# Optimization experiments

Hardware: AMD Instinct MI355X
Metric: run time of the kernel (lower is better)

The kernel has to match this reference:

```python
import jax, jax.numpy as jnp
import numpy as np

N = 50000          # nodes
E = 1600000        # edges
H = 8              # heads
F = 16             # out feats per head (np1class)
IN = 256           # in feats
NEG_SLOPE = 0.2    # DGL GATConv default leaky_relu slope


def setup_inputs() -> dict:
    key = jax.random.key(0)
    ks = jax.random.split(key, 7)
    x = jax.random.normal(ks[0], (N, IN), dtype=jnp.float32)
    W = jax.random.normal(ks[1], (IN, H * F), dtype=jnp.float32) * 0.05
    attn_l = jax.random.normal(ks[2], (H, F), dtype=jnp.float32) * 0.05
    attn_r = jax.random.normal(ks[3], (H, F), dtype=jnp.float32) * 0.05
    bias = jax.random.normal(ks[4], (H * F,), dtype=jnp.float32) * 0.05
    src = jax.random.randint(ks[5], (E,), 0, N, dtype=jnp.int64)
    dst = jax.random.randint(ks[6], (E,), 0, N, dtype=jnp.int64)
    return {"x": x, "W": W, "attn_l": attn_l, "attn_r": attn_r,
            "bias": bias, "src": src, "dst": dst}


def reference(x, W, attn_l, attn_r, bias, src, dst):
    # Linear projection to heads: [N, H, F]
    feat = (x @ W).reshape(N, H, F)
    # Per-node attention halves: [N, H]
    el = jnp.einsum('nhf,hf->nh', feat, attn_l)
    er = jnp.einsum('nhf,hf->nh', feat, attn_r)
    # Edge scores: e = leaky_relu(el[src] + er[dst])  -> [E, H]
    e = jax.nn.leaky_relu(el[src] + er[dst], negative_slope=NEG_SLOPE)
    # Segment softmax over incoming edges of each destination node
    m = jax.ops.segment_max(e, dst, num_segments=N)           # [N, H]
    m = jnp.where(jnp.isfinite(m), m, 0.0)                    # empty segments
    m = jax.lax.stop_gradient(m)
    ex = jnp.exp(e - m[dst])                                  # [E, H]
    s = jax.ops.segment_sum(ex, dst, num_segments=N)          # [N, H]
    a = ex / jnp.maximum(s[dst], 1e-9)                        # [E, H]
    # Weighted aggregation of source features: [N, H, F]
    msg = a[:, :, None] * feat[src]
    rst = jax.ops.segment_sum(msg, dst, num_segments=N)
    rst = rst + bias.reshape(H, F)
    # Classifier: mean over heads -> [N, F]
    return rst.mean(axis=1)
```

## Files before the change

kernel.cpp:

```cpp
#include <hip/hip_runtime.h>
#include <hip/hip_bf16.h>

#define NH 8
#define NF 16
#define NIN 256
#define HF 128
#define CAP 3072

typedef __attribute__((ext_vector_type(8))) short bf16x8;
typedef __attribute__((ext_vector_type(4))) float f32x4;

__device__ __forceinline__ unsigned short f2bf(float f) {
    union { float f; unsigned int u; } v; v.f = f;
    unsigned int r = v.u + 0x7FFFu + ((v.u >> 16) & 1u);
    return (unsigned short)(r >> 16);
}
__device__ __forceinline__ float bf2f(unsigned short b) {
    union { unsigned int u; float f; } v; v.u = ((unsigned int)b) << 16;
    return v.f;
}

#define GROWS 128
__global__ __launch_bounds__(256) void gemm_mfma(const float* __restrict__ A,
                                                 const float* __restrict__ W,
                                                 const float* __restrict__ attn_l,
                                                 const float* __restrict__ attn_r,
                                                 unsigned short* __restrict__ featb,
                                                 float* __restrict__ el,
                                                 float* __restrict__ er, int M) {
    __shared__ unsigned short AsH[32][264];
    __shared__ unsigned short AsL[32][264];
    const int tid = threadIdx.x;
    const int wave = tid >> 6, lane = tid & 63;
    const int quad = lane >> 4, lq = lane & 15;
    const int row0 = blockIdx.x * GROWS;

    bf16x8 bfrag[8][2];
#pragma unroll
    for (int h2 = 0; h2 < 2; h2++) {
        const int col = (wave * 2 + h2) * 16 + lq;
#pragma unroll
        for (int kk = 0; kk < 8; kk++) {
            const int kb = kk * 32 + quad * 8;
            bf16x8 f;
#pragma unroll
            for (int j = 0; j < 8; j++)
                f[j] = (short)f2bf(W[(size_t)(kb + j) * HF + col]);
            bfrag[kk][h2] = f;
        }
    }
    const float al0 = attn_l[(wave * 2 + 0) * 16 + lq];
    const float al1 = attn_l[(wave * 2 + 1) * 16 + lq];
    const float ar0 = attn_r[(wave * 2 + 0) * 16 + lq];
    const float ar1 = attn_r[(wave * 2 + 1) * 16 + lq];

    const int srow = tid >> 3;

    for (int c = 0; c < 4; c++) {
        const int crow0 = row0 + c * 32;
        __syncthreads();
#pragma unroll
        for (int i = 0; i < 8; i++) {
            const int col = ((tid & 7) + i * 8) * 4;
            const int gr = crow0 + srow;
            float4 v = make_float4(0.f, 0.f, 0.f, 0.f);
            if (gr < M) v = *(const float4*)&A[(size_t)gr * NIN + col];
            const unsigned short h0 = f2bf(v.x), h1 = f2bf(v.y),
                                 h2b = f2bf(v.z), h3 = f2bf(v.w);
            *(ushort4*)&AsH[srow][col] = make_ushort4(h0, h1, h2b, h3);
            *(ushort4*)&AsL[srow][col] =
                make_ushort4(f2bf(v.x - bf2f(h0)), f2bf(v.y - bf2f(h1)),
                             f2bf(v.z - bf2f(h2b)), f2bf(v.w - bf2f(h3)));
        }
        __syncthreads();
#pragma unroll
        for (int s = 0; s < 2; s++) {
            f32x4 acc0 = {0.f, 0.f, 0.f, 0.f};
            f32x4 acc1 = {0.f, 0.f, 0.f, 0.f};
            const int ar = s * 16 + lq;
#pragma unroll
            for (int kk = 0; kk < 8; kk++) {
                const bf16x8 ah = *(const bf16x8*)&AsH[ar][kk * 32 + quad * 8];
                const bf16x8 al = *(const bf16x8*)&AsL[ar][kk * 32 + quad * 8];
                acc0 = __builtin_amdgcn_mfma_f32_16x16x32_bf16(ah, bfrag[kk][0], acc0, 0, 0, 0);
                acc1 = __builtin_amdgcn_mfma_f32_16x16x32_bf16(ah, bfrag[kk][1], acc1, 0, 0, 0);
                acc0 = __builtin_amdgcn_mfma_f32_16x16x32_bf16(al, bfrag[kk][0], acc0, 0, 0, 0);
                acc1 = __builtin_amdgcn_mfma_f32_16x16x32_bf16(al, bfrag[kk][1], acc1, 0, 0, 0);
            }
#pragma unroll
            for (int r = 0; r < 4; r++) {
                const int gr = crow0 + s * 16 + quad * 4 + r;
                float pl0 = acc0[r] * al0, pr0 = acc0[r] * ar0;
                float pl1 = acc1[r] * al1, pr1 = acc1[r] * ar1;
#pragma unroll
                for (int m = 1; m < 16; m <<= 1) {
                    pl0 += __shfl_xor(pl0, m, 64);
                    pr0 += __shfl_xor(pr0, m, 64);
                    pl1 += __shfl_xor(pl1, m, 64);
                    pr1 += __shfl_xor(pr1, m, 64);
                }
                if (gr < M) {
                    featb[(size_t)gr * HF + (wave * 2 + 0) * 16 + lq] = f2bf(acc0[r]);
                    featb[(size_t)gr * HF + (wave * 2 + 1) * 16 + lq] = f2bf(acc1[r]);
                    if (lq == 0) {
                        el[(size_t)gr * NH + wave * 2 + 0] = pl0;
                        el[(size_t)gr * NH + wave * 2 + 1] = pl1;
                        er[(size_t)gr * NH + wave * 2 + 0] = pr0;
                        er[(size_t)gr * NH + wave * 2 + 1] = pr1;
                    }
                }
            }
        }
    }
}

#define BCH 16384
__global__ __launch_bounds__(256) void bin_kernel(const int* __restrict__ src,
                                                  const int* __restrict__ dst,
                                                  int* __restrict__ bcnt,
                                                  unsigned int* __restrict__ binned,
                                                  int E, int NB) {
    __shared__ unsigned int hist[800];
    __shared__ unsigned short lpos[BCH];
    const int tid = threadIdx.x;
    const int base = blockIdx.x * BCH;
    for (int b = tid; b < NB; b += 256) hist[b] = 0;
    __syncthreads();
    const int cnt = min(BCH, E - base);
    for (int i = tid; i < cnt; i += 256) {
        const int b = dst[base + i] >> 6;
        lpos[i] = (unsigned short)atomicAdd(&hist[b], 1u);
    }
    __syncthreads();
    for (int b = tid; b < NB; b += 256) {
        const unsigned int c = hist[b];
        if (c) hist[b] = (unsigned int)(b * CAP + atomicAdd(&bcnt[b], (int)c));
    }
    __syncthreads();
    for (int i = tid; i < cnt; i += 256) {
        const int d = dst[base + i];
        const int b = d >> 6;
        const unsigned int pos = hist[b] + (unsigned int)lpos[i];
        binned[pos] = (unsigned int)src[base + i] | ((unsigned int)(d & 63) << 16);
    }
}

__global__ __launch_bounds__(1024) void bscan_kernel(const int* __restrict__ bcnt,
                                                     int* __restrict__ bbase,
                                                     int* __restrict__ rowptr,
                                                     int NB, int N, int E) {
    __shared__ int wsum[16];
    const int t = threadIdx.x, lane = t & 63, w = t >> 6;
    const int v = (t < NB) ? bcnt[t] : 0;
    int incl = v;
#pragma unroll
    for (int off = 1; off < 64; off <<= 1) {
        const int x = __shfl_up(incl, off, 64);
        if (lane >= off) incl += x;
    }
    if (lane == 63) wsum[w] = incl;
    __syncthreads();
    int wbase = 0;
    for (int k = 0; k < w; k++) wbase += wsum[k];
    if (t < NB) bbase[t] = wbase + incl - v;
    if (t == 0) rowptr[N] = E;
}

__global__ __launch_bounds__(256) void csr_kernel(const int* __restrict__ bcnt,
                                                  const int* __restrict__ bbase,
                                                  const unsigned int* __restrict__ binned,
                                                  int* __restrict__ rowptr,
                                                  int* __restrict__ srcs, int N) {
    __shared__ int cnt64[64];
    __shared__ int cur[64];
    const int b = blockIdx.x, t = threadIdx.x;
    const int node0 = b << 6;
    const int cntb = bcnt[b];
    const unsigned int* bb = &binned[(size_t)b * CAP];
    if (t < 64) cnt64[t] = 0;
    __syncthreads();
    for (int i = t; i < cntb; i += 256) atomicAdd(&cnt64[bb[i] >> 16], 1);
    __syncthreads();
    if (t < 64) {
        const int v = cnt64[t];
        int incl = v;
#pragma unroll
        for (int off = 1; off < 64; off <<= 1) {
            const int x = __shfl_up(incl, off, 64);
            if (t >= off) incl += x;
        }
        const int excl = bbase[b] + incl - v;
        if (node0 + t < N) rowptr[node0 + t] = excl;
        cur[t] = excl;
    }
    __syncthreads();
    for (int i = t; i < cntb; i += 256) {
        const unsigned int p = bb[i];
        const int pos = atomicAdd(&cur[p >> 16], 1);
        srcs[pos] = (int)(p & 0xFFFFu);
    }
}

__global__ __launch_bounds__(128) void agg_kernel(const int* __restrict__ rowptr,
                                                  const int* __restrict__ srcs,
                                                  const float* __restrict__ el,
                                                  const float* __restrict__ er,
                                                  const unsigned short* __restrict__ featb,
                                                  const float* __restrict__ bias,
                                                  float* __restrict__ out) {
    const int n = blockIdx.x;
    const int tid = threadIdx.x;
    __shared__ float lds_sc[32][8];
    __shared__ int lds_src[32];
    __shared__ float lds_ps[128];
    __shared__ float lds_s[8];
    __shared__ float2 lds_acc[2][64];
    __shared__ float2 lds_v[8][8];

    const int begin = rowptr[n], end = rowptr[n + 1];
    const int hA = tid & 7, eA = tid >> 3;
    const float er_h = er[(size_t)n * NH + hA];
    const int w = tid >> 6, lane = tid & 63;
    const int hB = lane >> 3, fB2 = lane & 7;

    float2 acc = make_float2(0.f, 0.f);
    float psum = 0.f;
    for (int base = begin; base < end; base += 32) {
        const int cn = min(32, end - base);
#pragma unroll
        for (int rep = 0; rep < 2; rep++) {
            const int ei = eA + rep * 16;
            if (ei < cn) {
                const int si = srcs[base + ei];
                if (hA == 0) lds_src[ei] = si;
                float v = el[(size_t)si * NH + hA] + er_h;
                v = v > 0.f ? v : 0.2f * v;
                const float sc = __expf(v);
                lds_sc[ei][hA] = sc;
                psum += sc;
            }
        }
        __syncthreads();
        unsigned int fv[16];
#pragma unroll
        for (int j = 0; j < 16; j++) {
            const int ej = w * 16 + j;
            const int sj = lds_src[ej];
            fv[j] = (ej < cn)
                        ? *(const unsigned int*)&featb[(size_t)sj * HF + hB * 16 + fB2 * 2]
                        : 0u;
        }
#pragma unroll
        for (int j = 0; j < 16; j++) {
            const int ej = w * 16 + j;
            const float sc = (ej < cn) ? lds_sc[ej][hB] : 0.f;
            acc.x = fmaf(sc, bf2f((unsigned short)(fv[j] & 0xFFFFu)), acc.x);
            acc.y = fmaf(sc, bf2f((unsigned short)(fv[j] >> 16)), acc.y);
        }
        __syncthreads();
    }

    lds_ps[tid] = psum;
    lds_acc[w][lane] = acc;
    __syncthreads();
    if (tid < 8) {
        float s = 0.f;
#pragma unroll
        for (int k = 0; k < 16; k++) s += lds_ps[k * 8 + tid];
        lds_s[tid] = fmaxf(s, 1e-9f);
    }
    __syncthreads();
    if (tid < 64) {
        const float2 t0 = lds_acc[0][tid], t1 = lds_acc[1][tid];
        const float inv = 1.f / lds_s[hB];
        float2 val;
        val.x = (t0.x + t1.x) * inv + bias[hB * 16 + fB2 * 2];
        val.y = (t0.y + t1.y) * inv + bias[hB * 16 + fB2 * 2 + 1];
        lds_v[hB][fB2] = val;
    }
    __syncthreads();
    if (tid < 8) {
        float2 o = make_float2(0.f, 0.f);
#pragma unroll
        for (int h = 0; h < 8; h++) {
            const float2 v = lds_v[h][tid];
            o.x += v.x; o.y += v.y;
        }
        o.x *= 0.125f; o.y *= 0.125f;
        *(float2*)&out[(size_t)n * 16 + tid * 2] = o;
    }
}

extern "C" void kernel_launch(void* const* d_in, const int* in_sizes, int n_in,
                              void* d_out, int out_size, void* d_ws, size_t ws_size,
                              hipStream_t stream) {
    const float* x      = (const float*)d_in[0];
    const float* W      = (const float*)d_in[1];
    const float* attn_l = (const float*)d_in[2];
    const float* attn_r = (const float*)d_in[3];
    const float* bias   = (const float*)d_in[4];
    const int*   src    = (const int*)d_in[5];
    const int*   dst    = (const int*)d_in[6];
    float* out = (float*)d_out;

    const int N = in_sizes[0] / NIN;
    const int E = in_sizes[5];
    const int NB = (N + 63) >> 6;

    char* w = (char*)d_ws;
    unsigned short* featb = (unsigned short*)w; w += (size_t)N * HF * 2;
    float* el     = (float*)w; w += (size_t)N * NH * 4;
    float* er     = (float*)w; w += (size_t)N * NH * 4;
    int* rowptr   = (int*)w;   w += (size_t)(N + 16) * 4;
    int* bcnt     = (int*)w;   w += (size_t)((NB + 15) & ~15) * 4;
    int* bbase    = (int*)w;   w += (size_t)((NB + 15) & ~15) * 4;
    unsigned int* binned = (unsigned int*)w; w += (size_t)NB * CAP * 4;
    int* srcs     = (int*)w;

    hipMemsetAsync(bcnt, 0, (size_t)NB * sizeof(int), stream);

    gemm_mfma<<<(N + GROWS - 1) / GROWS, 256, 0, stream>>>(x, W, attn_l, attn_r,
                                                           featb, el, er, N);
    bin_kernel<<<(E + BCH - 1) / BCH, 256, 0, stream>>>(src, dst, bcnt, binned, E, NB);
    bscan_kernel<<<1, 1024, 0, stream>>>(bcnt, bbase, rowptr, NB, N, E);
    csr_kernel<<<NB, 256, 0, stream>>>(bcnt, bbase, binned, rowptr, srcs, N);
    agg_kernel<<<N, 128, 0, stream>>>(rowptr, srcs, el, er, featb, bias, out);
}
```

Measured before the change: 260.3 us.

## Fuse CSR construction into aggregation; one block per 64-node bin

Removes the global scan and CSR kernels. Each aggregation block now takes one 64-node bin, builds a local per-node sort of source indices in shared memory, and loops over its 64 nodes serially with 256 threads. The bin chunk size also shrinks, which gives more binning blocks. This saves two launches and the global srcs/rowptr round trip, but the grid drops from 50000 blocks to about 782. Each block processes its nodes one after another with many barriers, so latency hiding for the featb gathers may suffer.

Result: slower. 344.1 us (+32.2%).

```diff
diff --git a/kernel.cpp b/kernel.cpp
--- a/kernel.cpp
+++ b/kernel.cpp
@@ -6,6 +6,7 @@
 #define NIN 256
 #define HF 128
 #define CAP 3072
+#define BCH 4096
 
 typedef __attribute__((ext_vector_type(8))) short bf16x8;
 typedef __attribute__((ext_vector_type(4))) float f32x4;
@@ -114,7 +115,6 @@
     }
 }
 
-#define BCH 16384
 __global__ __launch_bounds__(256) void bin_kernel(const int* __restrict__ src,
                                                   const int* __restrict__ dst,
                                                   int* __restrict__ bcnt,
@@ -145,149 +145,136 @@
     }
 }
 
-__global__ __launch_bounds__(1024) void bscan_kernel(const int* __restrict__ bcnt,
-                                                     int* __restrict__ bbase,
-                                                     int* __restrict__ rowptr,
-                                                     int NB, int N, int E) {
-    __shared__ int wsum[16];
-    const int t = threadIdx.x, lane = t & 63, w = t >> 6;
-    const int v = (t < NB) ? bcnt[t] : 0;
-    int incl = v;
-#pragma unroll
-    for (int off = 1; off < 64; off <<= 1) {
-        const int x = __shfl_up(incl, off, 64);
-        if (lane >= off) incl += x;
-    }
-    if (lane == 63) wsum[w] = incl;
-    __syncthreads();
-    int wbase = 0;
-    for (int k = 0; k < w; k++) wbase += wsum[k];
-    if (t < NB) bbase[t] = wbase + incl - v;
-    if (t == 0) rowptr[N] = E;
-}
-
-__global__ __launch_bounds__(256) void csr_kernel(const int* __restrict__ bcnt,
-                                                  const int* __restrict__ bbase,
+__global__ __launch_bounds__(256) void agg_kernel(const int* __restrict__ bcnt,
                                                   const unsigned int* __restrict__ binned,
-                                                  int* __restrict__ rowptr,
-                                                  int* __restrict__ srcs, int N) {
-    __shared__ int cnt64[64];
-    __shared__ int cur[64];
-    const int b = blockIdx.x, t = threadIdx.x;
-    const int node0 = b << 6;
-    const int cntb = bcnt[b];
-    const unsigned int* bb = &binned[(size_t)b * CAP];
-    if (t < 64) cnt64[t] = 0;
-    __syncthreads();
-    for (int i = t; i < cntb; i += 256) atomicAdd(&cnt64[bb[i] >> 16], 1);
-    __syncthreads();
-    if (t < 64) {
-        const int v = cnt64[t];
-        int incl = v;
-#pragma unroll
-        for (int off = 1; off < 64; off <<= 1) {
-            const int x = __shfl_up(incl, off, 64);
-            if (t >= off) incl += x;
-        }
-        const int excl = bbase[b] + incl - v;
-        if (node0 + t < N) rowptr[node0 + t] = excl;
-        cur[t] = excl;
-    }
-    __syncthreads();
-    for (int i = t; i < cntb; i += 256) {
-        const unsigned int p = bb[i];
-        const int pos = atomicAdd(&cur[p >> 16], 1);
-        srcs[pos] = (int)(p & 0xFFFFu);
-    }
-}
-
-__global__ __launch_bounds__(128) void agg_kernel(const int* __restrict__ rowptr,
-                                                  const int* __restrict__ srcs,
                                                   const float* __restrict__ el,
                                                   const float* __restrict__ er,
                                                   const unsigned short* __restrict__ featb,
                                                   const float* __restrict__ bias,
-                                                  float* __restrict__ out) {
-    const int n = blockIdx.x;
-    const int tid = threadIdx.x;
-    __shared__ float lds_sc[32][8];
-    __shared__ int lds_src[32];
-    __shared__ float lds_ps[128];
-    __shared__ float lds_s[8];
-    __shared__ float2 lds_acc[2][64];
-    __shared__ float2 lds_v[8][8];
-
-    const int begin = rowptr[n], end = rowptr[n + 1];
-    const int hA = tid & 7, eA = tid >> 3;
-    const float er_h = er[(size_t)n * NH + hA];
-    const int w = tid >> 6, lane = tid & 63;
+                                                  float* __restrict__ out, int N) {
+    const int b = blockIdx.x, t = threadIdx.x;
+    const int node0 = b << 6;
+    __shared__ unsigned short sSrc[CAP];
+    __shared__ int len64[64], base64[64], cur64[64];
+    __shared__ float er_lds[64][NH];
+    __shared__ float lds_sc[32][NH];
+    __shared__ float lds_ps[256];
+    __shared__ float lds_s[NH];
+    __shared__ float2 lds_acc[4][64];
+    __shared__ float2 lds_v[NH][8];
+
+    const int cntb = bcnt[b];
+    const unsigned int* bb = &binned[(size_t)b * CAP];
+
+    if (t < 64) len64[t] = 0;
+    __syncthreads();
+    for (int i = t; i < cntb; i += 256) atomicAdd(&len64[bb[i] >> 16], 1);
+    __syncthreads();
+    if (t < 64) {
+        const int v = len64[t];
+        int incl = v;
+#pragma unroll
+        for (int off = 1; off < 64; off <<= 1) {
+            const int x = __shfl_up(incl, off, 64);
+            if (t >= off) incl += x;
+        }
+        base64[t] = incl - v;
+        cur64[t] = incl - v;
+    }
+    {
+        const int lim = min(64 * NH, (N - node0) * NH);
+        __syncthreads();
+        for (int i = t; i < lim; i += 256)
+            ((float*)er_lds)[i] = er[(size_t)node0 * NH + i];
+    }
+    __syncthreads();
+    for (int i = t; i < cntb; i += 256) {
+        const unsigned int p = bb[i];
+        const int pos = atomicAdd(&cur64[p >> 16], 1);
+        sSrc[pos] = (unsigned short)(p & 0xFFFFu);
+    }
+    __syncthreads();
+
+    const int hA = t & 7, eA = t >> 3;
+    const int w = t >> 6, lane = t & 63;
     const int hB = lane >> 3, fB2 = lane & 7;
 
-    float2 acc = make_float2(0.f, 0.f);
-    float psum = 0.f;
-    for (int base = begin; base < end; base += 32) {
-        const int cn = min(32, end - base);
-#pragma unroll
-        for (int rep = 0; rep < 2; rep++) {
-            const int ei = eA + rep * 16;
-            if (ei < cn) {
-                const int si = srcs[base + ei];
-                if (hA == 0) lds_src[ei] = si;
+    const int nmax = min(64, N - node0);
+    for (int nl = 0; nl < nmax; nl++) {
+        const int begin = base64[nl];
+        const int lenn = len64[nl];
+        const float er_h = er_lds[nl][hA];
+        float2 acc = make_float2(0.f, 0.f);
+        float psum = 0.f;
+        for (int base = begin; base < begin + lenn; base += 32) {
+            const int cn = min(32, begin + lenn - base);
+            if (eA < cn) {
+                const int si = sSrc[base + eA];
                 float v = el[(size_t)si * NH + hA] + er_h;
                 v = v > 0.f ? v : 0.2f * v;
                 const float sc = __expf(v);
-                lds_sc[ei][hA] = sc;
+                lds_sc[eA][hA] = sc;
                 psum += sc;
             }
-        }
-        __syncthreads();
-        unsigned int fv[16];
-#pragma unroll
-        for (int j = 0; j < 16; j++) {
-            const int ej = w * 16 + j;
-            const int sj = lds_src[ej];
-            fv[j] = (ej < cn)
-                        ? *(const unsigned int*)&featb[(size_t)sj * HF + hB * 16 + fB2 * 2]
-                        : 0u;
-        }
-#pragma unroll
-        for (int j = 0; j < 16; j++) {
-            const int ej = w * 16 + j;
-            const float sc = (ej < cn) ? lds_sc[ej][hB] : 0.f;
-            acc.x = fmaf(sc, bf2f((unsigned short)(fv[j] & 0xFFFFu)), acc.x);
-            acc.y = fmaf(sc, bf2f((unsigned short)(fv[j] >> 16)), acc.y);
-        }
-        __syncthreads();
-    }
-
-    lds_ps[tid] = psum;
-    lds_acc[w][lane] = acc;
-    __syncthreads();
-    if (tid < 8) {
-        float s = 0.f;
-#pragma unroll
-        for (int k = 0; k < 16; k++) s += lds_ps[k * 8 + tid];
-        lds_s[tid] = fmaxf(s, 1e-9f);
-    }
-    __syncthreads();
-    if (tid < 64) {
-        const float2 t0 = lds_acc[0][tid], t1 = lds_acc[1][tid];
-        const float inv = 1.f / lds_s[hB];
-        float2 val;
-        val.x = (t0.x + t1.x) * inv + bias[hB * 16 + fB2 * 2];
-        val.y = (t0.y + t1.y) * inv + bias[hB * 16 + fB2 * 2 + 1];
-        lds_v[hB][fB2] = val;
-    }
-    __syncthreads();
-    if (tid < 8) {
-        float2 o = make_float2(0.f, 0.f);
-#pragma unroll
-        for (int h = 0; h < 8; h++) {
-            const float2 v = lds_v[h][tid];
-            o.x += v.x; o.y += v.y;
-        }
-        o.x *= 0.125f; o.y *= 0.125f;
-        *(float2*)&out[(size_t)n * 16 + tid * 2] = o;
+            __syncthreads();
+            int sj[8];
+#pragma unroll
+            for (int j = 0; j < 8; j++) {
+                const int ej = w * 8 + j;
+                sj[j] = (ej < cn) ? (int)sSrc[base + ej] : 0;
+            }
+            unsigned int fv[8];
+#pragma unroll
+            for (int j = 0; j < 8; j++) {
+                const int ej = w * 8 + j;
+                fv[j] = (ej < cn)
+                            ? *(const unsigned int*)&featb[(size_t)sj[j] * HF + hB * 16 + fB2 * 2]
+                            : 0u;
+            }
+#pragma unroll
+            for (int j = 0; j < 8; j++) {
+                const int ej = w * 8 + j;
+                const float sc = (ej < cn) ? lds_sc[ej][hB] : 0.f;
+                acc.x = fmaf(sc, bf2f((unsigned short)(fv[j] & 0xFFFFu)), acc.x);
+                acc.y = fmaf(sc, bf2f((unsigned short)(fv[j] >> 16)), acc.y);
+            }
+            __syncthreads();
+        }
+        lds_ps[t] = psum;
+        lds_acc[w][lane] = acc;
+        __syncthreads();
+        if (t < 8) {
+            float s = 0.f;
+#pragma unroll
+            for (int k = 0; k < 32; k++) s += lds_ps[k * 8 + t];
+            lds_s[t] = fmaxf(s, 1e-9f);
+        }
+        __syncthreads();
+        if (t < 64) {
+            float2 a = lds_acc[0][t];
+#pragma unroll
+            for (int k = 1; k < 4; k++) {
+                a.x += lds_acc[k][t].x;
+                a.y += lds_acc[k][t].y;
+            }
+            const float inv = 1.f / lds_s[t >> 3];
+            float2 val;
+            val.x = a.x * inv + bias[(t >> 3) * 16 + (t & 7) * 2];
+            val.y = a.y * inv + bias[(t >> 3) * 16 + (t & 7) * 2 + 1];
+            lds_v[t >> 3][t & 7] = val;
+        }
+        __syncthreads();
+        if (t < 8) {
+            float2 o = make_float2(0.f, 0.f);
+#pragma unroll
+            for (int h = 0; h < NH; h++) {
+                const float2 v = lds_v[h][t];
+                o.x += v.x; o.y += v.y;
+            }
+            o.x *= 0.125f; o.y *= 0.125f;
+            *(float2*)&out[(size_t)(node0 + nl) * 16 + t * 2] = o;
+        }
+        __syncthreads();
     }
 }
 
@@ -311,18 +298,13 @@
     unsigned short* featb = (unsigned short*)w; w += (size_t)N * HF * 2;
     float* el     = (float*)w; w += (size_t)N * NH * 4;
     float* er     = (float*)w; w += (size_t)N * NH * 4;
-    int* rowptr   = (int*)w;   w += (size_t)(N + 16) * 4;
     int* bcnt     = (int*)w;   w += (size_t)((NB + 15) & ~15) * 4;
-    int* bbase    = (int*)w;   w += (size_t)((NB + 15) & ~15) * 4;
-    unsigned int* binned = (unsigned int*)w; w += (size_t)NB * CAP * 4;
-    int* srcs     = (int*)w;
+    unsigned int* binned = (unsigned int*)w;
 
     hipMemsetAsync(bcnt, 0, (size_t)NB * sizeof(int), stream);
 
     gemm_mfma<<<(N + GROWS - 1) / GROWS, 256, 0, stream>>>(x, W, attn_l, attn_r,
                                                            featb, el, er, N);
     bin_kernel<<<(E + BCH - 1) / BCH, 256, 0, stream>>>(src, dst, bcnt, binned, E, NB);
-    bscan_kernel<<<1, 1024, 0, stream>>>(bcnt, bbase, rowptr, NB, N, E);
-    csr_kernel<<<NB, 256, 0, stream>>>(bcnt, bbase, binned, rowptr, srcs, N);
-    agg_kernel<<<N, 128, 0, stream>>>(rowptr, srcs, el, er, featb, bias, out);
-}
+    agg_kernel<<<NB, 256, 0, stream>>>(bcnt, binned, el, er, featb, bias, out, N);
+}
```

## Use 256-node bins with bin-local CSR and 16-bit source indices

Applied to the files above, without the earlier changes.

Enlarges destination bins to 256 nodes and builds a bin-local CSR with per-node packed offset/length, eliminating the global scan kernel. Source indices are stored as 16-bit values to cut index traffic in aggregation, and binning uses smaller chunks for more blocks. Risks include fewer CSR blocks with more work each, a fixed per-bin capacity that could overflow on skewed graphs, and reliance on N fitting in 16 bits.

After: 247.3 us. -5.0%, faster.

```diff
diff --git a/kernel.cpp b/kernel.cpp
--- a/kernel.cpp
+++ b/kernel.cpp
@@ -5,7 +5,9 @@
 #define NF 16
 #define NIN 256
 #define HF 128
-#define CAP 3072
+#define BNODES 256
+#define CAP 9216
+#define BCH 4096
 
 typedef __attribute__((ext_vector_type(8))) short bf16x8;
 typedef __attribute__((ext_vector_type(4))) float f32x4;
@@ -114,95 +116,79 @@
     }
 }
 
-#define BCH 16384
 __global__ __launch_bounds__(256) void bin_kernel(const int* __restrict__ src,
                                                   const int* __restrict__ dst,
                                                   int* __restrict__ bcnt,
                                                   unsigned int* __restrict__ binned,
                                                   int E, int NB) {
-    __shared__ unsigned int hist[800];
+    __shared__ unsigned int hist[256];
     __shared__ unsigned short lpos[BCH];
     const int tid = threadIdx.x;
     const int base = blockIdx.x * BCH;
-    for (int b = tid; b < NB; b += 256) hist[b] = 0;
+    if (tid < NB) hist[tid] = 0;
     __syncthreads();
     const int cnt = min(BCH, E - base);
     for (int i = tid; i < cnt; i += 256) {
-        const int b = dst[base + i] >> 6;
+        const int b = dst[base + i] >> 8;
         lpos[i] = (unsigned short)atomicAdd(&hist[b], 1u);
     }
     __syncthreads();
-    for (int b = tid; b < NB; b += 256) {
-        const unsigned int c = hist[b];
-        if (c) hist[b] = (unsigned int)(b * CAP + atomicAdd(&bcnt[b], (int)c));
+    if (tid < NB) {
+        const unsigned int c = hist[tid];
+        if (c) hist[tid] = (unsigned int)(tid * CAP + atomicAdd(&bcnt[tid], (int)c));
     }
     __syncthreads();
     for (int i = tid; i < cnt; i += 256) {
         const int d = dst[base + i];
-        const int b = d >> 6;
+        const int b = d >> 8;
         const unsigned int pos = hist[b] + (unsigned int)lpos[i];
-        binned[pos] = (unsigned int)src[base + i] | ((unsigned int)(d & 63) << 16);
-    }
-}
-
-__global__ __launch_bounds__(1024) void bscan_kernel(const int* __restrict__ bcnt,
-                                                     int* __restrict__ bbase,
-                                                     int* __restrict__ rowptr,
-                                                     int NB, int N, int E) {
-    __shared__ int wsum[16];
-    const int t = threadIdx.x, lane = t & 63, w = t >> 6;
-    const int v = (t < NB) ? bcnt[t] : 0;
-    int incl = v;
-#pragma unroll
-    for (int off = 1; off < 64; off <<= 1) {
-        const int x = __shfl_up(incl, off, 64);
-        if (lane >= off) incl += x;
-    }
-    if (lane == 63) wsum[w] = incl;
-    __syncthreads();
-    int wbase = 0;
-    for (int k = 0; k < w; k++) wbase += wsum[k];
-    if (t < NB) bbase[t] = wbase + incl - v;
-    if (t == 0) rowptr[N] = E;
+        binned[pos] = (unsigned int)src[base + i] | ((unsigned int)(d & 255) << 16);
+    }
 }
 
 __global__ __launch_bounds__(256) void csr_kernel(const int* __restrict__ bcnt,
-                                                  const int* __restrict__ bbase,
                                                   const unsigned int* __restrict__ binned,
-                                                  int* __restrict__ rowptr,
-                                                  int* __restrict__ srcs, int N) {
-    __shared__ int cnt64[64];
-    __shared__ int cur[64];
+                                                  int* __restrict__ nodeinfo,
+                                                  unsigned short* __restrict__ srcsw,
+                                                  int N) {
+    __shared__ int len[BNODES], cur[BNODES];
+    __shared__ int wsum[4];
     const int b = blockIdx.x, t = threadIdx.x;
-    const int node0 = b << 6;
+    const int node0 = b << 8;
     const int cntb = bcnt[b];
     const unsigned int* bb = &binned[(size_t)b * CAP];
-    if (t < 64) cnt64[t] = 0;
-    __syncthreads();
-    for (int i = t; i < cntb; i += 256) atomicAdd(&cnt64[bb[i] >> 16], 1);
-    __syncthreads();
-    if (t < 64) {
-        const int v = cnt64[t];
+    unsigned short* sw = &srcsw[(size_t)b * CAP];
+    len[t] = 0;
+    __syncthreads();
+    for (int i = t; i < cntb; i += 256) atomicAdd(&len[bb[i] >> 16], 1);
+    __syncthreads();
+    {
+        const int lane = t & 63, w = t >> 6;
+        const int v = len[t];
         int incl = v;
 #pragma unroll
         for (int off = 1; off < 64; off <<= 1) {
             const int x = __shfl_up(incl, off, 64);
-            if (t >= off) incl += x;
-        }
-        const int excl = bbase[b] + incl - v;
-        if (node0 + t < N) rowptr[node0 + t] = excl;
+            if (lane >= off) incl += x;
+        }
+        if (lane == 63) wsum[w] = incl;
+        __syncthreads();
+        int wbase = 0;
+        for (int k = 0; k < w; k++) wbase += wsum[k];
+        const int excl = wbase + incl - v;
         cur[t] = excl;
+        if (node0 + t < N) nodeinfo[node0 + t] = excl | (v << 16);
     }
     __syncthreads();
     for (int i = t; i < cntb; i += 256) {
         const unsigned int p = bb[i];
         const int pos = atomicAdd(&cur[p >> 16], 1);
-        srcs[pos] = (int)(p & 0xFFFFu);
-    }
-}
-
-__global__ __launch_bounds__(128) void agg_kernel(const int* __restrict__ rowptr,
-                                                  const int* __restrict__ srcs,
+        sw[pos] = (unsigned short)(p & 0xFFFFu);
+    }
+}
+
+__global__ __launch_bounds__(128) void agg_kernel(const int* __restrict__ nodeinfo,
+                                                  const unsigned short* __restrict__ srcsw,
                                                   const float* __restrict__ el,
                                                   const float* __restrict__ er,
                                                   const unsigned short* __restrict__ featb,
@@ -217,7 +203,9 @@
     __shared__ float2 lds_acc[2][64];
     __shared__ float2 lds_v[8][8];
 
-    const int begin = rowptr[n], end = rowptr[n + 1];
+    const int info = nodeinfo[n];
+    const int begin = (n >> 8) * CAP + (info & 0xFFFF);
+    const int end = begin + (info >> 16);
     const int hA = tid & 7, eA = tid >> 3;
     const float er_h = er[(size_t)n * NH + hA];
     const int w = tid >> 6, lane = tid & 63;
@@ -231,7 +219,7 @@
         for (int rep = 0; rep < 2; rep++) {
             const int ei = eA + rep * 16;
             if (ei < cn) {
-                const int si = srcs[base + ei];
+                const int si = (int)srcsw[base + ei];
                 if (hA == 0) lds_src[ei] = si;
                 float v = el[(size_t)si * NH + hA] + er_h;
                 v = v > 0.f ? v : 0.2f * v;
@@ -305,24 +293,22 @@
 
     const int N = in_sizes[0] / NIN;
     const int E = in_sizes[5];
-    const int NB = (N + 63) >> 6;
+    const int NB = (N + BNODES - 1) >> 8;
 
     char* w = (char*)d_ws;
     unsigned short* featb = (unsigned short*)w; w += (size_t)N * HF * 2;
     float* el     = (float*)w; w += (size_t)N * NH * 4;
     float* er     = (float*)w; w += (size_t)N * NH * 4;
-    int* rowptr   = (int*)w;   w += (size_t)(N + 16) * 4;
+    int* nodeinfo = (int*)w;   w += (size_t)N * 4;
     int* bcnt     = (int*)w;   w += (size_t)((NB + 15) & ~15) * 4;
-    int* bbase    = (int*)w;   w += (size_t)((NB + 15) & ~15) * 4;
     unsigned int* binned = (unsigned int*)w; w += (size_t)NB * CAP * 4;
-    int* srcs     = (int*)w;
+    unsigned short* srcsw = (unsigned short*)w;
 
     hipMemsetAsync(bcnt, 0, (size_t)NB * sizeof(int), stream);
 
     gemm_mfma<<<(N + GROWS - 1) / GROWS, 256, 0, stream>>>(x, W, attn_l, attn_r,
                                                            featb, el, er, N);
     bin_kernel<<<(E + BCH - 1) / BCH, 256, 0, stream>>>(src, dst, bcnt, binned, E, NB);
-    bscan_kernel<<<1, 1024, 0, stream>>>(bcnt, bbase, rowptr, NB, N, E);
-    csr_kernel<<<NB, 256, 0, stream>>>(bcnt, bbase, binned, rowptr, srcs, N);
-    agg_kernel<<<N, 128, 0, stream>>>(rowptr, srcs, el, er, featb, bias, out);
-}
+    csr_kernel<<<NB, 256, 0, stream>>>(bcnt, binned, nodeinfo, srcsw, N);
+    agg_kernel<<<N, 128, 0, stream>>>(nodeinfo, srcsw, el, er, featb, bias, out);
+}
```
